# Kernel tuning notes

Measured on AMD Instinct MI355X. Metric: run time of the kernel, lower is better.

The kernel has to match this reference:

```python
import jax, jax.numpy as jnp
import numpy as np

HIDDEN = 1024
HEADS = 16
HEAD_DIM = HIDDEN // HEADS
B, S = 2, 2048


def setup_inputs() -> dict:
    key = jax.random.key(0)
    ks = jax.random.split(key, 9)
    sc = 1.0 / np.sqrt(HIDDEN)
    return {
        "hidden_state": jax.random.normal(ks[0], (B, S, HIDDEN), dtype=jnp.float32),
        "wq": jax.random.normal(ks[1], (HIDDEN, HIDDEN), dtype=jnp.float32) * sc,
        "bq": jax.random.normal(ks[2], (HIDDEN,), dtype=jnp.float32) * 0.01,
        "wk": jax.random.normal(ks[3], (HIDDEN, HIDDEN), dtype=jnp.float32) * sc,
        "bk": jax.random.normal(ks[4], (HIDDEN,), dtype=jnp.float32) * 0.01,
        "wv": jax.random.normal(ks[5], (HIDDEN, HIDDEN), dtype=jnp.float32) * sc,
        "bv": jax.random.normal(ks[6], (HIDDEN,), dtype=jnp.float32) * 0.01,
        "wo": jax.random.normal(ks[7], (HIDDEN, HIDDEN), dtype=jnp.float32) * sc,
        "bo": jax.random.normal(ks[8], (HIDDEN,), dtype=jnp.float32) * 0.01,
    }


def reference(hidden_state, wq, bq, wk, bk, wv, bv, wo, bo):
    b, s, _ = hidden_state.shape

    def split_head(x):  # [B,S,H*D] -> [B,H,S,D]
        return x.reshape(b, s, HEADS, HEAD_DIM).transpose(0, 2, 1, 3)

    q = split_head(hidden_state @ wq + bq)
    k = split_head(hidden_state @ wk + bk)
    v = split_head(hidden_state @ wv + bv)

    # NOTE: original scales by sqrt(hidden_size), NOT sqrt(head_dim)
    scale = 1.0 / jnp.sqrt(jnp.float32(HIDDEN))
    scores = jnp.einsum("bhqd,bhkd->bhqk", q, k) * scale  # [B,H,S,S]
    probs = jax.nn.softmax(scores, axis=-1)
    out = jnp.einsum("bhqk,bhkd->bhqd", probs, v)  # [B,H,S,D]

    # Faithful to source: transpose(-1,-2) then view (this is the original's
    # layout, which differs from the conventional transpose(1,2) merge)
    out = out.transpose(0, 1, 3, 2).reshape(b, -1, HEADS * HEAD_DIM)
    return out @ wo + bo
```

## Files before the change

### kernel.cpp

```cpp
#include <hip/hip_runtime.h>
#include <stdint.h>


typedef unsigned short u16;
typedef __bf16 bf16x8 __attribute__((ext_vector_type(8)));
typedef u16 u16x8 __attribute__((ext_vector_type(8)));
typedef u16 u16x4 __attribute__((ext_vector_type(4)));
typedef float f32x4 __attribute__((ext_vector_type(4)));

#define DEV static __device__ __forceinline__

DEV bf16x8 as_bf16x8(u16x8 u) { union { u16x8 u; bf16x8 b; } c; c.u = u; return c.b; }
DEV u16 f2bf(float f) {
  uint32_t u = __float_as_uint(f);
  u += 0x7fffu + ((u >> 16) & 1u);
  return (u16)(u >> 16);
}
DEV uint32_t pk_rhu(float a, float b) {
  uint32_t ua = __float_as_uint(a) + 0x8000u;
  uint32_t ub = __float_as_uint(b) + 0x8000u;
  return __builtin_amdgcn_perm(ub, ua, 0x07060302u);
}

DEV void gll16(const u16* g, u16* lds) {
  __builtin_amdgcn_global_load_lds((const __attribute__((address_space(1))) void*)g,
                                   (__attribute__((address_space(3))) void*)lds,
                                   16, 0, 0);
}

__global__ __launch_bounds__(256) void prep_kernel(
    const float* __restrict__ hid, const float* __restrict__ w0,
    const float* __restrict__ w1, const float* __restrict__ w2,
    const float* __restrict__ w3, u16* __restrict__ Ah,
    u16* __restrict__ Wt) {
  __shared__ __align__(16) float T[64][68];
  int bid = blockIdx.x, t = threadIdx.x;
  if (bid < 2048) {
    int i = (bid * 256 + t) * 8;
    f32x4 a = *(const f32x4*)&hid[i];
    f32x4 b = *(const f32x4*)&hid[i + 4];
    u16x8 o;
#pragma unroll
    for (int j = 0; j < 4; ++j) { o[j] = f2bf(a[j]); o[j + 4] = f2bf(b[j]); }
    *(u16x8*)&Ah[i] = o;
    return;
  }
  int tb = bid - 2048;
  int z = tb >> 8, rem = tb & 255;
  const float* W = (z == 0) ? w0 : (z == 1) ? w1 : (z == 2) ? w2 : w3;
  u16* O = Wt + (size_t)z * 1024 * 1024;
  int r0 = (rem >> 4) * 64, c0 = (rem & 15) * 64;
  int i = t >> 2, js = (t & 3) * 16;
#pragma unroll
  for (int jj = 0; jj < 16; jj += 4)
    *(f32x4*)&T[i][js + jj] = *(const f32x4*)&W[(size_t)(r0 + i) * 1024 + c0 + js + jj];
  __syncthreads();
#pragma unroll
  for (int seg = 0; seg < 2; ++seg) {
    u16x8 v;
#pragma unroll
    for (int jj = 0; jj < 8; ++jj) v[jj] = f2bf(T[js + seg * 8 + jj][i]);
    *(u16x8*)&O[(size_t)(c0 + i) * 1024 + r0 + js + seg * 8] = v;
  }
}

DEV void gemm_body(const u16* __restrict__ A, const u16* __restrict__ Bt,
                   const float* __restrict__ bias, u16* __restrict__ C,
                   int mode, float scale) {
  __shared__ __align__(16) u16 As[128 * 32], Bs[128 * 32];
  int tid = threadIdx.x, lane = tid & 63, w = tid >> 6;
  int quad = lane >> 4, l15 = lane & 15;
  int m0 = blockIdx.x * 128, n0 = blockIdx.y * 128;
  int wm = w >> 1, wn = w & 1;
  f32x4 acc[4][4] = {};

  for (int k0 = 0; k0 < 1024; k0 += 32) {
    __syncthreads();
#pragma unroll
    for (int i = 0; i < 2; ++i) {
      int idx = i * 256 + w * 64 + lane;
      int row = idx >> 2, cs = idx & 3, c = cs ^ ((row >> 1) & 3);
      gll16(A + (size_t)(m0 + row) * 1024 + k0 + c * 8, &As[(i * 256 + w * 64) * 8]);
      gll16(Bt + (size_t)(n0 + row) * 1024 + k0 + c * 8, &Bs[(i * 256 + w * 64) * 8]);
    }
    __syncthreads();
    bf16x8 af[4], bfr[4];
#pragma unroll
    for (int mt = 0; mt < 4; ++mt) {
      int row = wm * 64 + mt * 16 + l15;
      af[mt] = as_bf16x8(*(const u16x8*)&As[row * 32 + (quad ^ ((row >> 1) & 3)) * 8]);
    }
#pragma unroll
    for (int nt = 0; nt < 4; ++nt) {
      int row = wn * 64 + nt * 16 + l15;
      bfr[nt] = as_bf16x8(*(const u16x8*)&Bs[row * 32 + (quad ^ ((row >> 1) & 3)) * 8]);
    }
#pragma unroll
    for (int mt = 0; mt < 4; ++mt)
#pragma unroll
      for (int nt = 0; nt < 4; ++nt)
        acc[mt][nt] = __builtin_amdgcn_mfma_f32_16x16x32_bf16(af[mt], bfr[nt], acc[mt][nt], 0, 0, 0);
  }

#pragma unroll
  for (int nt = 0; nt < 4; ++nt) {
    int n = n0 + wn * 64 + nt * 16 + l15;
    float bv = bias[n];
#pragma unroll
    for (int mt = 0; mt < 4; ++mt) {
      int mbase = m0 + wm * 64 + mt * 16 + quad * 4;
      if (mode == 2) {
        int b = mbase >> 11, s = mbase & 2047, h = n >> 6, d = n & 63;
        size_t base = (((size_t)(b * 16 + h)) * 64 + d) * 2048 + s;
        u16x4 pk;
#pragma unroll
        for (int r = 0; r < 4; ++r) pk[r] = f2bf((acc[mt][nt][r] + bv) * scale);
        *(u16x4*)&C[base] = pk;
      } else {
#pragma unroll
        for (int r = 0; r < 4; ++r) {
          int m = mbase + r;
          int b = m >> 11, s = m & 2047, h = n >> 6, d = n & 63;
          C[(((size_t)(b * 16 + h)) * 2048 + s) * 64 + d] =
              f2bf((acc[mt][nt][r] + bv) * scale);
        }
      }
    }
  }
}

__global__ __launch_bounds__(256) void qkv_gemm(
    const u16* __restrict__ A, const u16* __restrict__ Wt,
    const float* __restrict__ bq, const float* __restrict__ bk,
    const float* __restrict__ bv, u16* __restrict__ Qb, u16* __restrict__ Kb,
    u16* __restrict__ Vt) {
  int z = blockIdx.z;
  const u16* Bt = Wt + (size_t)z * 1024 * 1024;
  const float* bias = (z == 0) ? bq : (z == 1) ? bk : bv;
  u16* C = (z == 0) ? Qb : (z == 1) ? Kb : Vt;
  gemm_body(A, Bt, bias, C, (z == 2) ? 2 : 1, (z == 0) ? 0.03125f : 1.0f);
}

__global__ __launch_bounds__(256) void out_gemm(
    const u16* __restrict__ A, const u16* __restrict__ Wt,
    const float* __restrict__ bo, float* __restrict__ C) {
  const u16* Bt = Wt + (size_t)3 * 1024 * 1024;
  __shared__ __align__(16) u16 As[64 * 32], Bs[128 * 32];
  int tid = threadIdx.x, lane = tid & 63, w = tid >> 6;
  int quad = lane >> 4, l15 = lane & 15;
  int m0 = blockIdx.x * 64, n0 = blockIdx.y * 128;
  f32x4 acc[4][2] = {};

  for (int k0 = 0; k0 < 1024; k0 += 32) {
    __syncthreads();
    {
      int idx = w * 64 + lane;
      int row = idx >> 2, cs = idx & 3, c = cs ^ ((row >> 1) & 3);
      gll16(A + (size_t)(m0 + row) * 1024 + k0 + c * 8, &As[(w * 64) * 8]);
#pragma unroll
      for (int i = 0; i < 2; ++i) {
        int bidx = i * 256 + w * 64 + lane;
        int brow = bidx >> 2, bcs = bidx & 3, bc = bcs ^ ((brow >> 1) & 3);
        gll16(Bt + (size_t)(n0 + brow) * 1024 + k0 + bc * 8,
              &Bs[(i * 256 + w * 64) * 8]);
      }
    }
    __syncthreads();
    bf16x8 af[4], bfr[2];
#pragma unroll
    for (int mt = 0; mt < 4; ++mt) {
      int row = mt * 16 + l15;
      af[mt] = as_bf16x8(*(const u16x8*)&As[row * 32 + (quad ^ ((row >> 1) & 3)) * 8]);
    }
#pragma unroll
    for (int nt = 0; nt < 2; ++nt) {
      int row = w * 32 + nt * 16 + l15;
      bfr[nt] = as_bf16x8(*(const u16x8*)&Bs[row * 32 + (quad ^ ((row >> 1) & 3)) * 8]);
    }
#pragma unroll
    for (int mt = 0; mt < 4; ++mt)
#pragma unroll
      for (int nt = 0; nt < 2; ++nt)
        acc[mt][nt] = __builtin_amdgcn_mfma_f32_16x16x32_bf16(af[mt], bfr[nt], acc[mt][nt], 0, 0, 0);
  }

#pragma unroll
  for (int nt = 0; nt < 2; ++nt) {
    int n = n0 + w * 32 + nt * 16 + l15;
    float bv = bo[n];
#pragma unroll
    for (int mt = 0; mt < 4; ++mt) {
      int mbase = m0 + mt * 16 + quad * 4;
#pragma unroll
      for (int r = 0; r < 4; ++r)
        C[(size_t)(mbase + r) * 1024 + n] = acc[mt][nt][r] + bv;
    }
  }
}

#define PSTR 72
__global__ __launch_bounds__(256, 2) void attn_kernel(
    const u16* __restrict__ Qb, const u16* __restrict__ Kb,
    const u16* __restrict__ Vtb, u16* __restrict__ Otb) {
  __shared__ __align__(16) u16 Ks[64 * PSTR], Vs[64 * PSTR];
  int tid = threadIdx.x, lane = tid & 63, w = tid >> 6;
  int quad = lane >> 4, l15 = lane & 15;
  int bh = blockIdx.x, q0 = blockIdx.y * 128;
  const size_t baseQK = (size_t)bh * 2048 * 64;

  bf16x8 bq[2][2];
#pragma unroll
  for (int g = 0; g < 2; ++g) {
    int qrow = q0 + w * 32 + g * 16 + l15;
#pragma unroll
    for (int ks = 0; ks < 2; ++ks)
      bq[g][ks] = as_bf16x8(*(const u16x8*)&Qb[baseQK + (size_t)qrow * 64 + (ks * 4 + quad) * 8]);
  }

  f32x4 o[2][4] = {};
  float l_run[2] = {0.0f, 0.0f};
  const int km = ((l15 & 12) << 1) | (l15 & 3);

  u16x8 tk[2], tv[2];
#pragma unroll
  for (int i = 0; i < 2; ++i) {
    int idx = i * 256 + tid;
    int row = idx >> 3, cs = idx & 7;
    tk[i] = *(const u16x8*)&Kb[baseQK + (size_t)row * 64 + cs * 8];
    tv[i] = *(const u16x8*)&Vtb[baseQK + (size_t)row * 2048 + cs * 8];
  }

  for (int kv = 0; kv < 32; ++kv) {
    __syncthreads();
#pragma unroll
    for (int i = 0; i < 2; ++i) {
      int idx = i * 256 + tid;
      int row = idx >> 3, cs = idx & 7;
      *(u16x8*)&Ks[row * PSTR + cs * 8] = tk[i];
      *(u16x8*)&Vs[row * PSTR + cs * 8] = tv[i];
    }
    __syncthreads();

    if (kv < 31) {
#pragma unroll
      for (int i = 0; i < 2; ++i) {
        int idx = i * 256 + tid;
        int row = idx >> 3, cs = idx & 7;
        tk[i] = *(const u16x8*)&Kb[baseQK + (size_t)((kv + 1) * 64 + row) * 64 + cs * 8];
        tv[i] = *(const u16x8*)&Vtb[baseQK + (size_t)row * 2048 + (kv + 1) * 64 + cs * 8];
      }
    }

    f32x4 scA[2][2] = {}, scB[2][2] = {};
    __builtin_amdgcn_s_setprio(1);
#pragma unroll
    for (int ks = 0; ks < 2; ++ks)
#pragma unroll
      for (int mtg = 0; mtg < 2; ++mtg) {
        bf16x8 akA = as_bf16x8(*(const u16x8*)&Ks[(mtg * 32 + km) * PSTR + (ks * 4 + quad) * 8]);
        bf16x8 akB = as_bf16x8(*(const u16x8*)&Ks[(mtg * 32 + km + 4) * PSTR + (ks * 4 + quad) * 8]);
#pragma unroll
        for (int g = 0; g < 2; ++g) {
          scA[g][mtg] = __builtin_amdgcn_mfma_f32_16x16x32_bf16(akA, bq[g][ks], scA[g][mtg], 0, 0, 0);
          scB[g][mtg] = __builtin_amdgcn_mfma_f32_16x16x32_bf16(akB, bq[g][ks], scB[g][mtg], 0, 0, 0);
        }
      }
    __builtin_amdgcn_s_setprio(0);

    bf16x8 bp[2][2];
#pragma unroll
    for (int g = 0; g < 2; ++g)
#pragma unroll
      for (int mtg = 0; mtg < 2; ++mtg) {
        float pA0 = __expf(scA[g][mtg][0] - 8.0f), pA1 = __expf(scA[g][mtg][1] - 8.0f);
        float pA2 = __expf(scA[g][mtg][2] - 8.0f), pA3 = __expf(scA[g][mtg][3] - 8.0f);
        float pB0 = __expf(scB[g][mtg][0] - 8.0f), pB1 = __expf(scB[g][mtg][1] - 8.0f);
        float pB2 = __expf(scB[g][mtg][2] - 8.0f), pB3 = __expf(scB[g][mtg][3] - 8.0f);
        l_run[g] += ((pA0 + pA1) + (pA2 + pA3)) + ((pB0 + pB1) + (pB2 + pB3));
        union { uint32_t u[4]; u16x8 v; } pk;
        pk.u[0] = pk_rhu(pA0, pA1);
        pk.u[1] = pk_rhu(pA2, pA3);
        pk.u[2] = pk_rhu(pB0, pB1);
        pk.u[3] = pk_rhu(pB2, pB3);
        bp[g][mtg] = as_bf16x8(pk.v);
      }

    __builtin_amdgcn_s_setprio(1);
#pragma unroll
    for (int mtg = 0; mtg < 2; ++mtg)
#pragma unroll
      for (int dt = 0; dt < 4; ++dt) {
        bf16x8 av = as_bf16x8(*(const u16x8*)&Vs[(dt * 16 + l15) * PSTR + (mtg * 4 + quad) * 8]);
#pragma unroll
        for (int g = 0; g < 2; ++g)
          o[g][dt] = __builtin_amdgcn_mfma_f32_16x16x32_bf16(av, bp[g][mtg], o[g][dt], 0, 0, 0);
      }
    __builtin_amdgcn_s_setprio(0);
  }

#pragma unroll
  for (int g = 0; g < 2; ++g) {
    l_run[g] += __shfl_xor(l_run[g], 16, 64);
    l_run[g] += __shfl_xor(l_run[g], 32, 64);
  }

#pragma unroll
  for (int g = 0; g < 2; ++g) {
    float inv = 1.0f / l_run[g];
#pragma unroll
    for (int dt = 0; dt < 4; ++dt)
#pragma unroll
      for (int r = 0; r < 4; ++r) {
        int d = dt * 16 + quad * 4 + r;
        Otb[(size_t)bh * 64 * 2048 + (size_t)d * 2048 + q0 + w * 32 + g * 16 + l15] =
            f2bf(o[g][dt][r] * inv);
      }
  }
}

extern "C" void kernel_launch(void* const* d_in, const int* in_sizes, int n_in,
                              void* d_out, int out_size, void* d_ws, size_t ws_size,
                              hipStream_t stream) {
  const float* hid = (const float*)d_in[0];
  const float* wq = (const float*)d_in[1];
  const float* bq = (const float*)d_in[2];
  const float* wk = (const float*)d_in[3];
  const float* bk = (const float*)d_in[4];
  const float* wv = (const float*)d_in[5];
  const float* bv = (const float*)d_in[6];
  const float* wo = (const float*)d_in[7];
  const float* bo = (const float*)d_in[8];

  u16* ws = (u16*)d_ws;
  const size_t MB2 = (size_t)1024 * 1024;
  u16* Wt  = ws;
  u16* Ah  = ws + 4 * MB2;
  u16* Qb  = ws + 8 * MB2;
  u16* Kb  = ws + 12 * MB2;
  u16* Vtb = ws + 16 * MB2;
  u16* Otb = Ah;

  prep_kernel<<<3072, 256, 0, stream>>>(hid, wq, wk, wv, wo, Ah, Wt);
  qkv_gemm<<<dim3(32, 8, 3), 256, 0, stream>>>(Ah, Wt, bq, bk, bv, Qb, Kb, Vtb);
  attn_kernel<<<dim3(32, 16), 256, 0, stream>>>(Qb, Kb, Vtb, Otb);
  out_gemm<<<dim3(64, 8), 256, 0, stream>>>(Otb, Wt, bo, (float*)d_out);
}
```

Before: 188.0 us.

## Double-buffer K/V shared tiles in attention kernel to drop one barrier per iteration

The attention loop now keeps two LDS buffers for K and V. The next tile is written into the idle buffer after the current tile's MFMAs finish, so each iteration needs one __syncthreads instead of two. The LDS row stride also changes from 72 to 80 elements, which alters the bank-conflict pattern. LDS use doubles to about 40 KB per block, which could limit occupancy relative to the two blocks requested per CU.

```diff
diff --git a/kernel.cpp b/kernel.cpp
--- a/kernel.cpp
+++ b/kernel.cpp
@@ -198,11 +198,11 @@
   }
 }
 
-#define PSTR 72
+#define PSTR 80
 __global__ __launch_bounds__(256, 2) void attn_kernel(
     const u16* __restrict__ Qb, const u16* __restrict__ Kb,
     const u16* __restrict__ Vtb, u16* __restrict__ Otb) {
-  __shared__ __align__(16) u16 Ks[64 * PSTR], Vs[64 * PSTR];
+  __shared__ __align__(16) u16 Ks[2][64 * PSTR], Vs[2][64 * PSTR];
   int tid = threadIdx.x, lane = tid & 63, w = tid >> 6;
   int quad = lane >> 4, l15 = lane & 15;
   int bh = blockIdx.x, q0 = blockIdx.y * 128;
@@ -220,35 +220,27 @@
   f32x4 o[2][4] = {};
   float l_run[2] = {0.0f, 0.0f};
   const int km = ((l15 & 12) << 1) | (l15 & 3);
+  const int srow = tid >> 3, scs = tid & 7;
+  const int srow2 = 32 + srow;
 
   u16x8 tk[2], tv[2];
-#pragma unroll
-  for (int i = 0; i < 2; ++i) {
-    int idx = i * 256 + tid;
-    int row = idx >> 3, cs = idx & 7;
-    tk[i] = *(const u16x8*)&Kb[baseQK + (size_t)row * 64 + cs * 8];
-    tv[i] = *(const u16x8*)&Vtb[baseQK + (size_t)row * 2048 + cs * 8];
-  }
+  tk[0] = *(const u16x8*)&Kb[baseQK + (size_t)srow * 64 + scs * 8];
+  tk[1] = *(const u16x8*)&Kb[baseQK + (size_t)srow2 * 64 + scs * 8];
+  tv[0] = *(const u16x8*)&Vtb[baseQK + (size_t)srow * 2048 + scs * 8];
+  tv[1] = *(const u16x8*)&Vtb[baseQK + (size_t)srow2 * 2048 + scs * 8];
+  *(u16x8*)&Ks[0][srow * PSTR + scs * 8] = tk[0];
+  *(u16x8*)&Ks[0][srow2 * PSTR + scs * 8] = tk[1];
+  *(u16x8*)&Vs[0][srow * PSTR + scs * 8] = tv[0];
+  *(u16x8*)&Vs[0][srow2 * PSTR + scs * 8] = tv[1];
+  __syncthreads();
 
   for (int kv = 0; kv < 32; ++kv) {
-    __syncthreads();
-#pragma unroll
-    for (int i = 0; i < 2; ++i) {
-      int idx = i * 256 + tid;
-      int row = idx >> 3, cs = idx & 7;
-      *(u16x8*)&Ks[row * PSTR + cs * 8] = tk[i];
-      *(u16x8*)&Vs[row * PSTR + cs * 8] = tv[i];
-    }
-    __syncthreads();
-
+    int cur = kv & 1;
     if (kv < 31) {
-#pragma unroll
-      for (int i = 0; i < 2; ++i) {
-        int idx = i * 256 + tid;
-        int row = idx >> 3, cs = idx & 7;
-        tk[i] = *(const u16x8*)&Kb[baseQK + (size_t)((kv + 1) * 64 + row) * 64 + cs * 8];
-        tv[i] = *(const u16x8*)&Vtb[baseQK + (size_t)row * 2048 + (kv + 1) * 64 + cs * 8];
-      }
+      tk[0] = *(const u16x8*)&Kb[baseQK + (size_t)((kv + 1) * 64 + srow) * 64 + scs * 8];
+      tk[1] = *(const u16x8*)&Kb[baseQK + (size_t)((kv + 1) * 64 + srow2) * 64 + scs * 8];
+      tv[0] = *(const u16x8*)&Vtb[baseQK + (size_t)srow * 2048 + (kv + 1) * 64 + scs * 8];
+      tv[1] = *(const u16x8*)&Vtb[baseQK + (size_t)srow2 * 2048 + (kv + 1) * 64 + scs * 8];
     }
 
     f32x4 scA[2][2] = {}, scB[2][2] = {};
@@ -257,8 +249,8 @@
     for (int ks = 0; ks < 2; ++ks)
 #pragma unroll
       for (int mtg = 0; mtg < 2; ++mtg) {
-        bf16x8 akA = as_bf16x8(*(const u16x8*)&Ks[(mtg * 32 + km) * PSTR + (ks * 4 + quad) * 8]);
-        bf16x8 akB = as_bf16x8(*(const u16x8*)&Ks[(mtg * 32 + km + 4) * PSTR + (ks * 4 + quad) * 8]);
+        bf16x8 akA = as_bf16x8(*(const u16x8*)&Ks[cur][(mtg * 32 + km) * PSTR + (ks * 4 + quad) * 8]);
+        bf16x8 akB = as_bf16x8(*(const u16x8*)&Ks[cur][(mtg * 32 + km + 4) * PSTR + (ks * 4 + quad) * 8]);
 #pragma unroll
         for (int g = 0; g < 2; ++g) {
           scA[g][mtg] = __builtin_amdgcn_mfma_f32_16x16x32_bf16(akA, bq[g][ks], scA[g][mtg], 0, 0, 0);
@@ -290,12 +282,21 @@
     for (int mtg = 0; mtg < 2; ++mtg)
 #pragma unroll
       for (int dt = 0; dt < 4; ++dt) {
-        bf16x8 av = as_bf16x8(*(const u16x8*)&Vs[(dt * 16 + l15) * PSTR + (mtg * 4 + quad) * 8]);
+        bf16x8 av = as_bf16x8(*(const u16x8*)&Vs[cur][(dt * 16 + l15) * PSTR + (mtg * 4 + quad) * 8]);
 #pragma unroll
         for (int g = 0; g < 2; ++g)
           o[g][dt] = __builtin_amdgcn_mfma_f32_16x16x32_bf16(av, bp[g][mtg], o[g][dt], 0, 0, 0);
       }
     __builtin_amdgcn_s_setprio(0);
+
+    if (kv < 31) {
+      int nb = cur ^ 1;
+      *(u16x8*)&Ks[nb][srow * PSTR + scs * 8] = tk[0];
+      *(u16x8*)&Ks[nb][srow2 * PSTR + scs * 8] = tk[1];
+      *(u16x8*)&Vs[nb][srow * PSTR + scs * 8] = tv[0];
+      *(u16x8*)&Vs[nb][srow2 * PSTR + scs * 8] = tv[1];
+    }
+    __syncthreads();
   }
 
 #pragma unroll
```

New measurement: 189.2 us. No clear change (+0.7%).

## Split attention KV range across two warp teams with double-buffered LDS

Applied to the files above, without the earlier changes.

The attention block doubles to 512 threads, organised as two teams of four waves. Each team processes half of the KV sequence for the same 128 queries. K/V tiles are double-buffered in LDS, so there is one barrier per iteration instead of two. At the end, team 1 writes its partial O and row sums to shared memory and team 0 combines them before normalizing, which is valid because the softmax uses a fixed max offset. This raises the number of waves in flight per query tile, at the cost of more LDS and a final reduction step.

```diff
diff --git a/kernel.cpp b/kernel.cpp
--- a/kernel.cpp
+++ b/kernel.cpp
@@ -198,15 +198,22 @@
   }
 }
 
-#define PSTR 72
-__global__ __launch_bounds__(256, 2) void attn_kernel(
+#define KSTR 80
+#define VSTR 72
+__global__ __launch_bounds__(512, 2) void attn_kernel(
     const u16* __restrict__ Qb, const u16* __restrict__ Kb,
     const u16* __restrict__ Vtb, u16* __restrict__ Otb) {
-  __shared__ __align__(16) u16 Ks[64 * PSTR], Vs[64 * PSTR];
-  int tid = threadIdx.x, lane = tid & 63, w = tid >> 6;
+  constexpr int KSZ = 64 * KSTR, VSZ = 64 * VSTR;
+  constexpr int TEAMSZ = 2 * (KSZ + VSZ);
+  __shared__ __align__(16) u16 smem[2 * TEAMSZ];
+  int tid = threadIdx.x;
+  int team = tid >> 8, tt = tid & 255;
+  int lane = tid & 63, w = (tid >> 6) & 3;
   int quad = lane >> 4, l15 = lane & 15;
   int bh = blockIdx.x, q0 = blockIdx.y * 128;
   const size_t baseQK = (size_t)bh * 2048 * 64;
+  u16* Ksb = smem + team * TEAMSZ;
+  u16* Vsb = smem + team * TEAMSZ + 2 * KSZ;
 
   bf16x8 bq[2][2];
 #pragma unroll
@@ -220,35 +227,31 @@
   f32x4 o[2][4] = {};
   float l_run[2] = {0.0f, 0.0f};
   const int km = ((l15 & 12) << 1) | (l15 & 3);
+  const int srow = tt >> 3, scs = tt & 7;
+  const int srow2 = 32 + srow;
+  const int kvbase = team * 16;
 
   u16x8 tk[2], tv[2];
-#pragma unroll
-  for (int i = 0; i < 2; ++i) {
-    int idx = i * 256 + tid;
-    int row = idx >> 3, cs = idx & 7;
-    tk[i] = *(const u16x8*)&Kb[baseQK + (size_t)row * 64 + cs * 8];
-    tv[i] = *(const u16x8*)&Vtb[baseQK + (size_t)row * 2048 + cs * 8];
-  }
-
-  for (int kv = 0; kv < 32; ++kv) {
-    __syncthreads();
-#pragma unroll
-    for (int i = 0; i < 2; ++i) {
-      int idx = i * 256 + tid;
-      int row = idx >> 3, cs = idx & 7;
-      *(u16x8*)&Ks[row * PSTR + cs * 8] = tk[i];
-      *(u16x8*)&Vs[row * PSTR + cs * 8] = tv[i];
-    }
-    __syncthreads();
-
-    if (kv < 31) {
-#pragma unroll
-      for (int i = 0; i < 2; ++i) {
-        int idx = i * 256 + tid;
-        int row = idx >> 3, cs = idx & 7;
-        tk[i] = *(const u16x8*)&Kb[baseQK + (size_t)((kv + 1) * 64 + row) * 64 + cs * 8];
-        tv[i] = *(const u16x8*)&Vtb[baseQK + (size_t)row * 2048 + (kv + 1) * 64 + cs * 8];
-      }
+  tk[0] = *(const u16x8*)&Kb[baseQK + (size_t)(kvbase * 64 + srow) * 64 + scs * 8];
+  tk[1] = *(const u16x8*)&Kb[baseQK + (size_t)(kvbase * 64 + srow2) * 64 + scs * 8];
+  tv[0] = *(const u16x8*)&Vtb[baseQK + (size_t)srow * 2048 + kvbase * 64 + scs * 8];
+  tv[1] = *(const u16x8*)&Vtb[baseQK + (size_t)srow2 * 2048 + kvbase * 64 + scs * 8];
+  *(u16x8*)&Ksb[srow * KSTR + scs * 8] = tk[0];
+  *(u16x8*)&Ksb[srow2 * KSTR + scs * 8] = tk[1];
+  *(u16x8*)&Vsb[srow * VSTR + scs * 8] = tv[0];
+  *(u16x8*)&Vsb[srow2 * VSTR + scs * 8] = tv[1];
+  __syncthreads();
+
+  for (int it = 0; it < 16; ++it) {
+    int cur = it & 1;
+    const u16* Kc = Ksb + cur * KSZ;
+    const u16* Vc = Vsb + cur * VSZ;
+    if (it < 15) {
+      int kv1 = kvbase + it + 1;
+      tk[0] = *(const u16x8*)&Kb[baseQK + (size_t)(kv1 * 64 + srow) * 64 + scs * 8];
+      tk[1] = *(const u16x8*)&Kb[baseQK + (size_t)(kv1 * 64 + srow2) * 64 + scs * 8];
+      tv[0] = *(const u16x8*)&Vtb[baseQK + (size_t)srow * 2048 + kv1 * 64 + scs * 8];
+      tv[1] = *(const u16x8*)&Vtb[baseQK + (size_t)srow2 * 2048 + kv1 * 64 + scs * 8];
     }
 
     f32x4 scA[2][2] = {}, scB[2][2] = {};
@@ -257,8 +260,8 @@
     for (int ks = 0; ks < 2; ++ks)
 #pragma unroll
       for (int mtg = 0; mtg < 2; ++mtg) {
-        bf16x8 akA = as_bf16x8(*(const u16x8*)&Ks[(mtg * 32 + km) * PSTR + (ks * 4 + quad) * 8]);
-        bf16x8 akB = as_bf16x8(*(const u16x8*)&Ks[(mtg * 32 + km + 4) * PSTR + (ks * 4 + quad) * 8]);
+        bf16x8 akA = as_bf16x8(*(const u16x8*)&Kc[(mtg * 32 + km) * KSTR + (ks * 4 + quad) * 8]);
+        bf16x8 akB = as_bf16x8(*(const u16x8*)&Kc[(mtg * 32 + km + 4) * KSTR + (ks * 4 + quad) * 8]);
 #pragma unroll
         for (int g = 0; g < 2; ++g) {
           scA[g][mtg] = __builtin_amdgcn_mfma_f32_16x16x32_bf16(akA, bq[g][ks], scA[g][mtg], 0, 0, 0);
@@ -290,12 +293,21 @@
     for (int mtg = 0; mtg < 2; ++mtg)
 #pragma unroll
       for (int dt = 0; dt < 4; ++dt) {
-        bf16x8 av = as_bf16x8(*(const u16x8*)&Vs[(dt * 16 + l15) * PSTR + (mtg * 4 + quad) * 8]);
+        bf16x8 av = as_bf16x8(*(const u16x8*)&Vc[(dt * 16 + l15) * VSTR + (mtg * 4 + quad) * 8]);
 #pragma unroll
         for (int g = 0; g < 2; ++g)
           o[g][dt] = __builtin_amdgcn_mfma_f32_16x16x32_bf16(av, bp[g][mtg], o[g][dt], 0, 0, 0);
       }
     __builtin_amdgcn_s_setprio(0);
+
+    if (it < 15) {
+      int nb = cur ^ 1;
+      *(u16x8*)&Ksb[nb * KSZ + srow * KSTR + scs * 8] = tk[0];
+      *(u16x8*)&Ksb[nb * KSZ + srow2 * KSTR + scs * 8] = tk[1];
+      *(u16x8*)&Vsb[nb * VSZ + srow * VSTR + scs * 8] = tv[0];
+      *(u16x8*)&Vsb[nb * VSTR * 0 + nb * VSZ + srow2 * VSTR + scs * 8] = tv[1];
+    }
+    __syncthreads();
   }
 
 #pragma unroll
@@ -304,17 +316,35 @@
     l_run[g] += __shfl_xor(l_run[g], 32, 64);
   }
 
-#pragma unroll
-  for (int g = 0; g < 2; ++g) {
-    float inv = 1.0f / l_run[g];
-#pragma unroll
-    for (int dt = 0; dt < 4; ++dt)
-#pragma unroll
-      for (int r = 0; r < 4; ++r) {
-        int d = dt * 16 + quad * 4 + r;
-        Otb[(size_t)bh * 64 * 2048 + (size_t)d * 2048 + q0 + w * 32 + g * 16 + l15] =
-            f2bf(o[g][dt][r] * inv);
-      }
+  float* Or = (float*)smem;
+  float* Lr = (float*)smem + 128 * 68;
+  if (team == 1) {
+#pragma unroll
+    for (int g = 0; g < 2; ++g) {
+      int q = w * 32 + g * 16 + l15;
+      if (quad == 0) Lr[q] = l_run[g];
+#pragma unroll
+      for (int dt = 0; dt < 4; ++dt)
+        *(f32x4*)&Or[q * 68 + dt * 16 + quad * 4] = o[g][dt];
+    }
+  }
+  __syncthreads();
+  if (team == 0) {
+#pragma unroll
+    for (int g = 0; g < 2; ++g) {
+      int q = w * 32 + g * 16 + l15;
+      float inv = 1.0f / (l_run[g] + Lr[q]);
+#pragma unroll
+      for (int dt = 0; dt < 4; ++dt) {
+        f32x4 ov = *(const f32x4*)&Or[q * 68 + dt * 16 + quad * 4];
+#pragma unroll
+        for (int r = 0; r < 4; ++r) {
+          int d = dt * 16 + quad * 4 + r;
+          Otb[(size_t)bh * 64 * 2048 + (size_t)d * 2048 + q0 + q] =
+              f2bf((o[g][dt][r] + ov[r]) * inv);
+        }
+      }
+    }
   }
 }
 
@@ -342,6 +372,6 @@
 
   prep_kernel<<<3072, 256, 0, stream>>>(hid, wq, wk, wv, wo, Ah, Wt);
   qkv_gemm<<<dim3(32, 8, 3), 256, 0, stream>>>(Ah, Wt, bq, bk, bv, Qb, Kb, Vtb);
-  attn_kernel<<<dim3(32, 16), 256, 0, stream>>>(Qb, Kb, Vtb, Otb);
+  attn_kernel<<<dim3(32, 16), 512, 0, stream>>>(Qb, Kb, Vtb, Otb);
   out_gemm<<<dim3(64, 8), 256, 0, stream>>>(Otb, Wt, bo, (float*)d_out);
 }
```

Measured after the change: 197.8 us. 5.2% more time.

## Load K/V fragments directly into registers and compute row sums via MFMA

Applied to the files above, without the earlier changes.

Drops the LDS staging of K and V tiles and the two block barriers per iteration. Each wave now loads its own MFMA operand fragments straight from global memory into registers, prefetching the next tile after each use. Folds log2(e) into the Q scale so the softmax uses a raw exp2 without the max offset, and accumulates the softmax denominator with an extra MFMA against a ones vector instead of scalar adds and shuffles. Each of the four waves now fetches the K/V data itself rather than sharing it through LDS, which multiplies global/L2 traffic. Dropping the constant offset also changes numerical headroom in the exponent.

```diff
diff --git a/kernel.cpp b/kernel.cpp
--- a/kernel.cpp
+++ b/kernel.cpp
@@ -16,11 +16,11 @@
   u += 0x7fffu + ((u >> 16) & 1u);
   return (u16)(u >> 16);
 }
-DEV uint32_t pk_rhu(float a, float b) {
-  uint32_t ua = __float_as_uint(a) + 0x8000u;
-  uint32_t ub = __float_as_uint(b) + 0x8000u;
-  return __builtin_amdgcn_perm(ub, ua, 0x07060302u);
-}
+#if __has_builtin(__builtin_amdgcn_exp2f)
+DEV float ex2(float x) { return __builtin_amdgcn_exp2f(x); }
+#else
+DEV float ex2(float x) { return exp2f(x); }
+#endif
 
 DEV void gll16(const u16* g, u16* lds) {
   __builtin_amdgcn_global_load_lds((const __attribute__((address_space(1))) void*)g,
@@ -138,7 +138,7 @@
   const u16* Bt = Wt + (size_t)z * 1024 * 1024;
   const float* bias = (z == 0) ? bq : (z == 1) ? bk : bv;
   u16* C = (z == 0) ? Qb : (z == 1) ? Kb : Vt;
-  gemm_body(A, Bt, bias, C, (z == 2) ? 2 : 1, (z == 0) ? 0.03125f : 1.0f);
+  gemm_body(A, Bt, bias, C, (z == 2) ? 2 : 1, (z == 0) ? 0.045084220f : 1.0f);
 }
 
 __global__ __launch_bounds__(256) void out_gemm(
@@ -198,15 +198,15 @@
   }
 }
 
-#define PSTR 72
 __global__ __launch_bounds__(256, 2) void attn_kernel(
     const u16* __restrict__ Qb, const u16* __restrict__ Kb,
     const u16* __restrict__ Vtb, u16* __restrict__ Otb) {
-  __shared__ __align__(16) u16 Ks[64 * PSTR], Vs[64 * PSTR];
   int tid = threadIdx.x, lane = tid & 63, w = tid >> 6;
   int quad = lane >> 4, l15 = lane & 15;
   int bh = blockIdx.x, q0 = blockIdx.y * 128;
   const size_t baseQK = (size_t)bh * 2048 * 64;
+  const u16* kbase = Kb + baseQK;
+  const u16* vbase = Vtb + baseQK;
 
   bf16x8 bq[2][2];
 #pragma unroll
@@ -217,72 +217,74 @@
       bq[g][ks] = as_bf16x8(*(const u16x8*)&Qb[baseQK + (size_t)qrow * 64 + (ks * 4 + quad) * 8]);
   }
 
+  bf16x8 av1;
+  {
+    u16x8 o1;
+#pragma unroll
+    for (int j = 0; j < 8; ++j) o1[j] = 0x3F80;
+    av1 = as_bf16x8(o1);
+  }
+
   f32x4 o[2][4] = {};
-  float l_run[2] = {0.0f, 0.0f};
+  f32x4 l_acc[2] = {};
   const int km = ((l15 & 12) << 1) | (l15 & 3);
 
-  u16x8 tk[2], tv[2];
-#pragma unroll
-  for (int i = 0; i < 2; ++i) {
-    int idx = i * 256 + tid;
-    int row = idx >> 3, cs = idx & 7;
-    tk[i] = *(const u16x8*)&Kb[baseQK + (size_t)row * 64 + cs * 8];
-    tv[i] = *(const u16x8*)&Vtb[baseQK + (size_t)row * 2048 + cs * 8];
-  }
+  u16x8 kA[2][2], kB[2][2];
+  u16x8 vv[2][4];
+
+#pragma unroll
+  for (int ks = 0; ks < 2; ++ks)
+#pragma unroll
+    for (int mtg = 0; mtg < 2; ++mtg) {
+      kA[ks][mtg] = *(const u16x8*)&kbase[(size_t)(mtg * 32 + km) * 64 + (ks * 4 + quad) * 8];
+      kB[ks][mtg] = *(const u16x8*)&kbase[(size_t)(mtg * 32 + km + 4) * 64 + (ks * 4 + quad) * 8];
+    }
+#pragma unroll
+  for (int mtg = 0; mtg < 2; ++mtg)
+#pragma unroll
+    for (int dt = 0; dt < 4; ++dt)
+      vv[mtg][dt] = *(const u16x8*)&vbase[(size_t)(dt * 16 + l15) * 2048 + mtg * 32 + quad * 8];
 
   for (int kv = 0; kv < 32; ++kv) {
-    __syncthreads();
-#pragma unroll
-    for (int i = 0; i < 2; ++i) {
-      int idx = i * 256 + tid;
-      int row = idx >> 3, cs = idx & 7;
-      *(u16x8*)&Ks[row * PSTR + cs * 8] = tk[i];
-      *(u16x8*)&Vs[row * PSTR + cs * 8] = tv[i];
-    }
-    __syncthreads();
-
-    if (kv < 31) {
-#pragma unroll
-      for (int i = 0; i < 2; ++i) {
-        int idx = i * 256 + tid;
-        int row = idx >> 3, cs = idx & 7;
-        tk[i] = *(const u16x8*)&Kb[baseQK + (size_t)((kv + 1) * 64 + row) * 64 + cs * 8];
-        tv[i] = *(const u16x8*)&Vtb[baseQK + (size_t)row * 2048 + (kv + 1) * 64 + cs * 8];
-      }
-    }
-
     f32x4 scA[2][2] = {}, scB[2][2] = {};
     __builtin_amdgcn_s_setprio(1);
 #pragma unroll
     for (int ks = 0; ks < 2; ++ks)
 #pragma unroll
       for (int mtg = 0; mtg < 2; ++mtg) {
-        bf16x8 akA = as_bf16x8(*(const u16x8*)&Ks[(mtg * 32 + km) * PSTR + (ks * 4 + quad) * 8]);
-        bf16x8 akB = as_bf16x8(*(const u16x8*)&Ks[(mtg * 32 + km + 4) * PSTR + (ks * 4 + quad) * 8]);
+        bf16x8 a0 = as_bf16x8(kA[ks][mtg]);
+        bf16x8 a1 = as_bf16x8(kB[ks][mtg]);
 #pragma unroll
         for (int g = 0; g < 2; ++g) {
-          scA[g][mtg] = __builtin_amdgcn_mfma_f32_16x16x32_bf16(akA, bq[g][ks], scA[g][mtg], 0, 0, 0);
-          scB[g][mtg] = __builtin_amdgcn_mfma_f32_16x16x32_bf16(akB, bq[g][ks], scB[g][mtg], 0, 0, 0);
+          scA[g][mtg] = __builtin_amdgcn_mfma_f32_16x16x32_bf16(a0, bq[g][ks], scA[g][mtg], 0, 0, 0);
+          scB[g][mtg] = __builtin_amdgcn_mfma_f32_16x16x32_bf16(a1, bq[g][ks], scB[g][mtg], 0, 0, 0);
         }
       }
     __builtin_amdgcn_s_setprio(0);
 
+    if (kv < 31) {
+      const u16* kp = kbase + (size_t)(kv + 1) * 64 * 64;
+#pragma unroll
+      for (int ks = 0; ks < 2; ++ks)
+#pragma unroll
+        for (int mtg = 0; mtg < 2; ++mtg) {
+          kA[ks][mtg] = *(const u16x8*)&kp[(size_t)(mtg * 32 + km) * 64 + (ks * 4 + quad) * 8];
+          kB[ks][mtg] = *(const u16x8*)&kp[(size_t)(mtg * 32 + km + 4) * 64 + (ks * 4 + quad) * 8];
+        }
+    }
+
     bf16x8 bp[2][2];
 #pragma unroll
     for (int g = 0; g < 2; ++g)
 #pragma unroll
       for (int mtg = 0; mtg < 2; ++mtg) {
-        float pA0 = __expf(scA[g][mtg][0] - 8.0f), pA1 = __expf(scA[g][mtg][1] - 8.0f);
-        float pA2 = __expf(scA[g][mtg][2] - 8.0f), pA3 = __expf(scA[g][mtg][3] - 8.0f);
-        float pB0 = __expf(scB[g][mtg][0] - 8.0f), pB1 = __expf(scB[g][mtg][1] - 8.0f);
-        float pB2 = __expf(scB[g][mtg][2] - 8.0f), pB3 = __expf(scB[g][mtg][3] - 8.0f);
-        l_run[g] += ((pA0 + pA1) + (pA2 + pA3)) + ((pB0 + pB1) + (pB2 + pB3));
-        union { uint32_t u[4]; u16x8 v; } pk;
-        pk.u[0] = pk_rhu(pA0, pA1);
-        pk.u[1] = pk_rhu(pA2, pA3);
-        pk.u[2] = pk_rhu(pB0, pB1);
-        pk.u[3] = pk_rhu(pB2, pB3);
-        bp[g][mtg] = as_bf16x8(pk.v);
+        float pA0 = ex2(scA[g][mtg][0]), pA1 = ex2(scA[g][mtg][1]);
+        float pA2 = ex2(scA[g][mtg][2]), pA3 = ex2(scA[g][mtg][3]);
+        float pB0 = ex2(scB[g][mtg][0]), pB1 = ex2(scB[g][mtg][1]);
+        float pB2 = ex2(scB[g][mtg][2]), pB3 = ex2(scB[g][mtg][3]);
+        bp[g][mtg] = (bf16x8){(__bf16)pA0, (__bf16)pA1, (__bf16)pA2, (__bf16)pA3,
+                              (__bf16)pB0, (__bf16)pB1, (__bf16)pB2, (__bf16)pB3};
+        l_acc[g] = __builtin_amdgcn_mfma_f32_16x16x32_bf16(av1, bp[g][mtg], l_acc[g], 0, 0, 0);
       }
 
     __builtin_amdgcn_s_setprio(1);
@@ -290,23 +292,26 @@
     for (int mtg = 0; mtg < 2; ++mtg)
 #pragma unroll
       for (int dt = 0; dt < 4; ++dt) {
-        bf16x8 av = as_bf16x8(*(const u16x8*)&Vs[(dt * 16 + l15) * PSTR + (mtg * 4 + quad) * 8]);
+        bf16x8 av = as_bf16x8(vv[mtg][dt]);
 #pragma unroll
         for (int g = 0; g < 2; ++g)
           o[g][dt] = __builtin_amdgcn_mfma_f32_16x16x32_bf16(av, bp[g][mtg], o[g][dt], 0, 0, 0);
       }
     __builtin_amdgcn_s_setprio(0);
+
+    if (kv < 31) {
+      const u16* vp = vbase + (size_t)(kv + 1) * 64;
+#pragma unroll
+      for (int mtg = 0; mtg < 2; ++mtg)
+#pragma unroll
+        for (int dt = 0; dt < 4; ++dt)
+          vv[mtg][dt] = *(const u16x8*)&vp[(size_t)(dt * 16 + l15) * 2048 + mtg * 32 + quad * 8];
+    }
   }
 
 #pragma unroll
   for (int g = 0; g < 2; ++g) {
-    l_run[g] += __shfl_xor(l_run[g], 16, 64);
-    l_run[g] += __shfl_xor(l_run[g], 32, 64);
-  }
-
-#pragma unroll
-  for (int g = 0; g < 2; ++g) {
-    float inv = 1.0f / l_run[g];
+    float inv = 1.0f / l_acc[g][0];
 #pragma unroll
     for (int dt = 0; dt < 4; ++dt)
 #pragma unroll
```

Result: slower. 258.3 us (+37.4%).
